# Optimization experiments

Measured on AMD Instinct MI355X. Metric: run time of the kernel, lower is better.

## Reference

```python
import jax, jax.numpy as jnp
import numpy as np

D_CHAR, D_HID, LEN_VOC = 256, 1024, 512
BSZ, MAX_LEN = 128, 256


def setup_inputs() -> dict:
    key = jax.random.key(0)
    ks = jax.random.split(key, 14)
    s = 1.0 / np.sqrt(D_HID)  # PyTorch RNN/Linear init scale
    u = lambda k, shape: jax.random.uniform(k, shape, jnp.float32, -s, s)
    return {
        "inputs": jax.random.randint(ks[0], (BSZ, MAX_LEN), 0, LEN_VOC),
        "outputs": jax.random.randint(ks[1], (BSZ, MAX_LEN), 0, LEN_VOC),
        "emb": jax.random.normal(ks[2], (LEN_VOC, D_CHAR), jnp.float32),
        "enc_Wih": u(ks[3], (D_HID, D_CHAR)),
        "enc_Whh": u(ks[4], (D_HID, D_HID)),
        "enc_bih": u(ks[5], (D_HID,)),
        "enc_bhh": u(ks[6], (D_HID,)),
        "dec_Wih": u(ks[7], (D_HID, D_CHAR)),
        "dec_Whh": u(ks[8], (D_HID, D_HID)),
        "dec_bih": u(ks[9], (D_HID,)),
        "dec_bhh": u(ks[10], (D_HID,)),
        "out_W": u(ks[11], (LEN_VOC, D_HID)),
        "out_b": u(ks[12], (LEN_VOC,)),
    }


def rnn_scan(x_seq, h0, Wih, Whh, bih, bhh):
    """Elman RNN (tanh), batch_first input [B, T, D] -> (h_T [B,H], all h [T,B,H]).
    h_t = tanh(W_ih x_t + b_ih + W_hh h_{t-1} + b_hh), matching torch.nn.RNN."""
    # Precompute input projection for all timesteps (one big GEMM).
    xp = jnp.einsum('btd,hd->bth', x_seq, Wih) + bih + bhh  # [B,T,H]
    xp = jnp.swapaxes(xp, 0, 1)  # [T,B,H] for scan

    def step(h, x):
        h = jnp.tanh(x + h @ Whh.T)
        return h, h

    hT, hs = jax.lax.scan(step, h0, xp)
    return hT, hs


def reference(inputs, outputs, emb, enc_Wih, enc_Whh, enc_bih, enc_bhh,
              dec_Wih, dec_Whh, dec_bih, dec_bhh, out_W, out_b):
    bsz, max_len = inputs.shape
    # Encoder over input char embeddings, zero initial hidden.
    embs = emb[inputs]  # [B,T,Dc]
    h0 = jnp.zeros((bsz, D_HID), jnp.float32)
    hT, _ = rnn_scan(embs, h0, enc_Wih, enc_Whh, enc_bih, enc_bhh)
    # Teacher-forced decoder: step 0 gets zero input, step t gets emb(outputs[:, t-1]).
    dec_in = jnp.concatenate(
        [jnp.zeros((bsz, 1, D_CHAR), jnp.float32), emb[outputs[:, :-1]]], axis=1)
    _, dec_hs = rnn_scan(dec_in, hT, dec_Wih, dec_Whh, dec_bih, dec_bhh)  # [T,B,H]
    # decoder_states.transpose(0,1).view(-1, d_hid)
    states = jnp.swapaxes(dec_hs, 0, 1).reshape(-1, D_HID)  # [B*T, H]
    logits = states @ out_W.T + out_b  # [B*T, V]
    return jax.nn.log_softmax(logits, axis=1)
```

## Files before the change

kernel.cpp:

```cpp
#include <hip/hip_runtime.h>


typedef short short8 __attribute__((ext_vector_type(8)));
typedef float floatx4 __attribute__((ext_vector_type(4)));
typedef unsigned int uint4v __attribute__((ext_vector_type(4)));

#define WS_HBUF   0ull
#define WS_STATES (2ull << 20)
#define WS_WB     (66ull << 20)

#define HS_STRIDE 1032

__device__ __forceinline__ float bf2f(unsigned short u) {
  union { unsigned u; float f; } x; x.u = ((unsigned)u) << 16; return x.f;
}
__device__ __forceinline__ unsigned short f2bf(float f) {
  union { float f; unsigned u; } x; x.f = f;
  unsigned r = x.u + 0x7FFFu + ((x.u >> 16) & 1u);
  return (unsigned short)(r >> 16);
}

__global__ __launch_bounds__(256) void cvt_kernel(
    const float* __restrict__ src, unsigned short* __restrict__ dst, int n)
{
  const int i = (blockIdx.x * 256 + threadIdx.x) * 4;
  if (i >= n) return;
  const float4 v = *(const float4*)(src + i);
  unsigned short o[4] = {f2bf(v.x), f2bf(v.y), f2bf(v.z), f2bf(v.w)};
  *(uint2*)(dst + i) = *(const uint2*)o;
}

__global__ __launch_bounds__(256) void gemm_bt_kernel(
    const unsigned short* __restrict__ Abase,
    const int mode,
    const unsigned short* __restrict__ Bmat,
    const float* __restrict__ bias0,
    const float* __restrict__ bias1,
    unsigned short* __restrict__ outp_bf,
    float* __restrict__ outp_f,
    const int K, const int N, const int nbn)
{
  __shared__ unsigned short As[64][264];
  __shared__ unsigned short Bs[64][264];
  __shared__ const unsigned short* rowsrc[64];

  const int tid = threadIdx.x;
  const int lane = tid & 63;
  const int wave = tid >> 6;
  const int bn = blockIdx.x % nbn;
  const int bm = blockIdx.x / nbn;
  const int m0 = bm * 64;
  const int j0 = bn * 64;

  if (tid < 64) {
    const int m = m0 + tid;
    const unsigned short* src;
    if (mode == 0) {
      src = Abase + (size_t)m * K;
    } else {
      src = Abase + ((size_t)(m & 255) * 128 + (m >> 8)) * 1024;
    }
    rowsrc[tid] = src;
  }

  const floatx4 zf = {0.f, 0.f, 0.f, 0.f};
  floatx4 acc0 = zf, acc1 = zf, acc2 = zf, acc3 = zf;

  for (int kc = 0; kc < K; kc += 256) {
    __syncthreads();
#pragma unroll
    for (int i = 0; i < 8; ++i) {
      const int idx = i * 256 + tid;
      const int r = idx >> 5;
      const int c = idx & 31;
      const unsigned short* s = rowsrc[r];
      *(short8*)&As[r][c * 8] = *(const short8*)(s + kc + c * 8);
      *(short8*)&Bs[r][c * 8] =
          *(const short8*)(Bmat + (size_t)(j0 + r) * K + kc + c * 8);
    }
    __syncthreads();
    const int ar = 16 * wave + (lane & 15);
    const int kq = (lane >> 4) * 8;
#pragma unroll
    for (int kk = 0; kk < 8; ++kk) {
      const short8 a = *(const short8*)&As[ar][kk * 32 + kq];
      const short8 bv0 = *(const short8*)&Bs[(lane & 15)][kk * 32 + kq];
      acc0 = __builtin_amdgcn_mfma_f32_16x16x32_bf16(a, bv0, acc0, 0, 0, 0);
      const short8 bv1 = *(const short8*)&Bs[16 + (lane & 15)][kk * 32 + kq];
      acc1 = __builtin_amdgcn_mfma_f32_16x16x32_bf16(a, bv1, acc1, 0, 0, 0);
      const short8 bv2 = *(const short8*)&Bs[32 + (lane & 15)][kk * 32 + kq];
      acc2 = __builtin_amdgcn_mfma_f32_16x16x32_bf16(a, bv2, acc2, 0, 0, 0);
      const short8 bv3 = *(const short8*)&Bs[48 + (lane & 15)][kk * 32 + kq];
      acc3 = __builtin_amdgcn_mfma_f32_16x16x32_bf16(a, bv3, acc3, 0, 0, 0);
    }
  }

  float bs[4] = {0.f, 0.f, 0.f, 0.f};
  if (bias0) {
#pragma unroll
    for (int nt = 0; nt < 4; ++nt) {
      const int jj = j0 + nt * 16 + (lane & 15);
      bs[nt] = bias0[jj] + bias1[jj];
    }
  }
  __syncthreads();
  const int rbase = 16 * wave + (lane >> 4) * 4;
  const int cl = lane & 15;

  if (outp_bf) {
#pragma unroll
    for (int i = 0; i < 4; ++i) {
      As[rbase + i][cl]      = f2bf(acc0[i] + bs[0]);
      As[rbase + i][16 + cl] = f2bf(acc1[i] + bs[1]);
      As[rbase + i][32 + cl] = f2bf(acc2[i] + bs[2]);
      As[rbase + i][48 + cl] = f2bf(acc3[i] + bs[3]);
    }
    __syncthreads();
#pragma unroll
    for (int i = 0; i < 2; ++i) {
      const int idx = i * 256 + tid;
      const int r = idx >> 3;
      const int c = idx & 7;
      *(short8*)(outp_bf + (size_t)(m0 + r) * N + j0 + c * 8) =
          *(const short8*)&As[r][c * 8];
    }
  } else {
    float (*Asf)[66] = (float(*)[66]) & As[0][0];
#pragma unroll
    for (int i = 0; i < 4; ++i) {
      Asf[rbase + i][cl]      = acc0[i] + bs[0];
      Asf[rbase + i][16 + cl] = acc1[i] + bs[1];
      Asf[rbase + i][32 + cl] = acc2[i] + bs[2];
      Asf[rbase + i][48 + cl] = acc3[i] + bs[3];
    }
    __syncthreads();
#pragma unroll
    for (int i = 0; i < 4; ++i) {
      const int idx = i * 256 + tid;
      const int r = idx >> 4;
      const int c = idx & 15;
      *(float4*)(outp_f + (size_t)(m0 + r) * N + j0 + c * 4) =
          *(const float4*)&Asf[r][c * 4];
    }
  }
}

__global__ __launch_bounds__(256) void rnn_scan8_kernel(
    const unsigned short* __restrict__ WhhE,
    const unsigned short* __restrict__ WhhD,
    const unsigned short* __restrict__ projE,
    const unsigned short* __restrict__ projD,
    const float* __restrict__ decBih,
    const float* __restrict__ decBhh,
    const int* __restrict__ intoks,
    const int* __restrict__ outtoks,
    unsigned short* __restrict__ hbuf,
    unsigned short* __restrict__ states,
    unsigned int* __restrict__ flags)
{
  __shared__ unsigned short hs[2 * 16 * HS_STRIDE];
  __shared__ int toks[16 * 257];

  const int tid = threadIdx.x;
  const int lane = tid & 63;
  const int wave = tid >> 6;
  const int g = blockIdx.x & 7;
  const int slot = blockIdx.x >> 3;
  const int b0 = g * 16;
  const int q = lane >> 4;
  const int cl = lane & 15;
  const int jwb = slot * 64 + wave * 16;
  const int jq4 = jwb + q * 4;
  unsigned int* grpflags = flags + (size_t)g * 1024;
  const int myflag = (slot * 4 + wave) * 16;

  short8 w[32];
  const floatx4 zf = {0.f, 0.f, 0.f, 0.f};
  const size_t prodoff = (size_t)(b0 + cl) * 1024 + jq4;

  for (int phase = 0; phase < 2; ++phase) {
    const unsigned short* Whh = phase ? WhhD : WhhE;
    const unsigned short* proj = phase ? projD : projE;
    const int* gt = phase ? outtoks : intoks;
    {
      const unsigned short* wp = Whh + (size_t)(jwb + cl) * 1024 + q * 8;
#pragma unroll
      for (int kk = 0; kk < 32; ++kk) w[kk] = *(const short8*)(wp + kk * 32);
    }
    float xb[4] = {0.f, 0.f, 0.f, 0.f};
    if (phase) {
#pragma unroll
      for (int i = 0; i < 4; ++i) xb[i] = decBih[jq4 + i] + decBhh[jq4 + i];
    }
    __syncthreads();
#pragma unroll
    for (int i = 0; i < 16; ++i) {
      const int idx = i * 256 + tid;
      toks[(idx >> 8) * 257 + (idx & 255)] =
          gt[(size_t)(b0 + (idx >> 8)) * 256 + (idx & 255)];
    }
    __syncthreads();

    for (int t = 0; t < 256; ++t) {
      const int s = phase * 256 + t;
      float xpf[4];
      {
        const int tt = phase ? (t > 0 ? t - 1 : 0) : t;
        const int tok = toks[cl * 257 + tt];
        const uint2 xr = *(const uint2*)(proj + (size_t)tok * 1024 + jq4);
        const unsigned short* xs = (const unsigned short*)&xr;
#pragma unroll
        for (int i = 0; i < 4; ++i) xpf[i] = bf2f(xs[i]);
        if (phase && t == 0) {
#pragma unroll
          for (int i = 0; i < 4; ++i) xpf[i] = xb[i];
        }
      }

      unsigned short* hsb = hs + (s & 1) * (16 * HS_STRIDE);
      if (s > 0) {
        const unsigned target = (unsigned)s;
        for (;;) {
          const unsigned f = __hip_atomic_load(&grpflags[lane * 16],
                                               __ATOMIC_RELAXED,
                                               __HIP_MEMORY_SCOPE_AGENT);
          if (__ballot(f < target) == 0ull) break;
          __builtin_amdgcn_s_sleep(1);
        }
        const unsigned short* hrb = hbuf + (size_t)(s & 1) * 131072 + b0 * 1024;
        uint4v p0, p1, p2, p3, p4, p5, p6, p7;
        {
          const unsigned long long a0 = (unsigned long long)(hrb + tid * 8);
          asm volatile(
              "global_load_dwordx4 %0, %8, off sc0 sc1\n\t"
              "global_load_dwordx4 %1, %9, off sc0 sc1\n\t"
              "global_load_dwordx4 %2, %10, off sc0 sc1\n\t"
              "global_load_dwordx4 %3, %11, off sc0 sc1\n\t"
              "global_load_dwordx4 %4, %12, off sc0 sc1\n\t"
              "global_load_dwordx4 %5, %13, off sc0 sc1\n\t"
              "global_load_dwordx4 %6, %14, off sc0 sc1\n\t"
              "global_load_dwordx4 %7, %15, off sc0 sc1\n\t"
              "s_waitcnt vmcnt(0)"
              : "=&v"(p0), "=&v"(p1), "=&v"(p2), "=&v"(p3),
                "=&v"(p4), "=&v"(p5), "=&v"(p6), "=&v"(p7)
              : "v"(a0),            "v"(a0 + 1 * 4096),
                "v"(a0 + 2 * 4096), "v"(a0 + 3 * 4096),
                "v"(a0 + 4 * 4096), "v"(a0 + 5 * 4096),
                "v"(a0 + 6 * 4096), "v"(a0 + 7 * 4096)
              : "memory");
        }
        __builtin_amdgcn_sched_barrier(0);
        {
          uint4v pp[8] = {p0, p1, p2, p3, p4, p5, p6, p7};
#pragma unroll
          for (int c = 0; c < 8; ++c) {
            const int gg = c * 256 + tid;
            *(uint4v*)&hsb[(gg >> 7) * HS_STRIDE + (gg & 127) * 8] = pp[c];
          }
        }
      }
      __builtin_amdgcn_sched_barrier(0);
      asm volatile("s_waitcnt lgkmcnt(0)" ::: "memory");
      __builtin_amdgcn_s_barrier();
      __builtin_amdgcn_sched_barrier(0);
      __builtin_amdgcn_s_setprio(1);

      floatx4 acc0 = zf, acc1 = zf, acc2 = zf, acc3 = zf;
      if (s > 0) {
        const unsigned short* hrow = &hsb[cl * HS_STRIDE + q * 8];
#pragma unroll
        for (int kk = 0; kk < 32; kk += 4) {
          const short8 a0 = *(const short8*)(hrow + (kk + 0) * 32);
          const short8 a1 = *(const short8*)(hrow + (kk + 1) * 32);
          const short8 a2 = *(const short8*)(hrow + (kk + 2) * 32);
          const short8 a3 = *(const short8*)(hrow + (kk + 3) * 32);
          acc0 = __builtin_amdgcn_mfma_f32_16x16x32_bf16(w[kk + 0], a0, acc0, 0, 0, 0);
          acc1 = __builtin_amdgcn_mfma_f32_16x16x32_bf16(w[kk + 1], a1, acc1, 0, 0, 0);
          acc2 = __builtin_amdgcn_mfma_f32_16x16x32_bf16(w[kk + 2], a2, acc2, 0, 0, 0);
          acc3 = __builtin_amdgcn_mfma_f32_16x16x32_bf16(w[kk + 3], a3, acc3, 0, 0, 0);
        }
      }
      unsigned short ob[4];
#pragma unroll
      for (int i = 0; i < 4; ++i) {
        const float pre = acc0[i] + acc1[i] + acc2[i] + acc3[i] + xpf[i];
        const float e = __expf(2.f * pre);
        ob[i] = f2bf(1.f - 2.f / (e + 1.f));
      }
      const unsigned long long obp = *(const unsigned long long*)ob;
      __hip_atomic_store(
          (unsigned long long*)(hbuf + (size_t)((s + 1) & 1) * 131072 + prodoff),
          obp, __ATOMIC_RELAXED, __HIP_MEMORY_SCOPE_AGENT);
      asm volatile("s_waitcnt vmcnt(0)" ::: "memory");
      if (lane == 0)
        __hip_atomic_store(&grpflags[myflag], (unsigned)(s + 1),
                           __ATOMIC_RELAXED, __HIP_MEMORY_SCOPE_AGENT);
      __builtin_amdgcn_s_setprio(0);
      if (phase) {
        __builtin_nontemporal_store(
            obp, (unsigned long long*)(states + (size_t)t * 131072 + prodoff));
      }
    }
  }
}

__global__ __launch_bounds__(256) void logsoftmax_kernel(
    float* __restrict__ logits, const float* __restrict__ outb)
{
  const int row = blockIdx.x * 4 + (threadIdx.x >> 6);
  const int lane = threadIdx.x & 63;
  float* rp = logits + (size_t)row * 512 + lane * 8;
  const float4 a0 = *(const float4*)rp;
  const float4 a1 = *(const float4*)(rp + 4);
  const float4 b0 = *(const float4*)(outb + lane * 8);
  const float4 b1 = *(const float4*)(outb + lane * 8 + 4);
  float v[8] = {a0.x + b0.x, a0.y + b0.y, a0.z + b0.z, a0.w + b0.w,
                a1.x + b1.x, a1.y + b1.y, a1.z + b1.z, a1.w + b1.w};
  float mx = v[0];
#pragma unroll
  for (int i = 1; i < 8; ++i) mx = fmaxf(mx, v[i]);
#pragma unroll
  for (int m = 1; m < 64; m <<= 1) mx = fmaxf(mx, __shfl_xor(mx, m, 64));
  float sum = 0.f;
#pragma unroll
  for (int i = 0; i < 8; ++i) sum += __expf(v[i] - mx);
#pragma unroll
  for (int m = 1; m < 64; m <<= 1) sum += __shfl_xor(sum, m, 64);
  const float lse = mx + __logf(sum);
  float4 o0 = {v[0] - lse, v[1] - lse, v[2] - lse, v[3] - lse};
  float4 o1 = {v[4] - lse, v[5] - lse, v[6] - lse, v[7] - lse};
  *(float4*)rp = o0;
  *(float4*)(rp + 4) = o1;
}

extern "C" void kernel_launch(void* const* d_in, const int* in_sizes, int n_in,
                              void* d_out, int out_size, void* d_ws, size_t ws_size,
                              hipStream_t stream)
{
  const int* inputs  = (const int*)d_in[0];
  const int* outputs = (const int*)d_in[1];
  const float* emb    = (const float*)d_in[2];
  const float* encWih = (const float*)d_in[3];
  const float* encWhh = (const float*)d_in[4];
  const float* encBih = (const float*)d_in[5];
  const float* encBhh = (const float*)d_in[6];
  const float* decWih = (const float*)d_in[7];
  const float* decWhh = (const float*)d_in[8];
  const float* decBih = (const float*)d_in[9];
  const float* decBhh = (const float*)d_in[10];
  const float* outW   = (const float*)d_in[11];
  const float* outB   = (const float*)d_in[12];

  char* ws = (char*)d_ws;
  unsigned short* hbuf   = (unsigned short*)(ws + WS_HBUF);
  unsigned short* states = (unsigned short*)(ws + WS_STATES);
  char* wb = ws + WS_WB;
  unsigned short* embB  = (unsigned short*)(wb + 0);
  unsigned short* eWihB = (unsigned short*)(wb + (512ull << 10));
  unsigned short* dWihB = (unsigned short*)(wb + (1ull << 20));
  unsigned short* eWhhB = (unsigned short*)(wb + (2ull << 20));
  unsigned short* dWhhB = (unsigned short*)(wb + (4ull << 20));
  unsigned short* outWB = (unsigned short*)(wb + (6ull << 20));
  unsigned short* projE = (unsigned short*)(wb + (7ull << 20));
  unsigned short* projD = (unsigned short*)(wb + (8ull << 20));
  unsigned int*   flags = (unsigned int*)  (wb + (9ull << 20));
  float* logits = (float*)d_out;

  hipMemsetAsync(flags, 0, 8 * 1024 * sizeof(unsigned int), stream);

  cvt_kernel<<<128, 256, 0, stream>>>(emb, embB, 512 * 256);
  cvt_kernel<<<256, 256, 0, stream>>>(encWih, eWihB, 1024 * 256);
  cvt_kernel<<<256, 256, 0, stream>>>(decWih, dWihB, 1024 * 256);
  cvt_kernel<<<1024, 256, 0, stream>>>(encWhh, eWhhB, 1024 * 1024);
  cvt_kernel<<<1024, 256, 0, stream>>>(decWhh, dWhhB, 1024 * 1024);
  cvt_kernel<<<512, 256, 0, stream>>>(outW, outWB, 512 * 1024);

  gemm_bt_kernel<<<128, 256, 0, stream>>>(embB, 0, eWihB, encBih, encBhh,
                                          projE, nullptr, 256, 1024, 16);
  gemm_bt_kernel<<<128, 256, 0, stream>>>(embB, 0, dWihB, decBih, decBhh,
                                          projD, nullptr, 256, 1024, 16);

  rnn_scan8_kernel<<<128, 256, 0, stream>>>(eWhhB, dWhhB, projE, projD,
                                            decBih, decBhh, inputs, outputs,
                                            hbuf, states, flags);

  gemm_bt_kernel<<<4096, 256, 0, stream>>>(states, 3, outWB, nullptr, nullptr,
                                           nullptr, logits, 1024, 512, 8);
  logsoftmax_kernel<<<8192, 256, 0, stream>>>(logits, outB);
}
```

Before: 1.624 ms.

## Fuse output projection GEMM with bias and log-softmax in one kernel

Replaces the separate output GEMM (64x64 tiles) and log-softmax pass with a kernel where each block computes full 512-wide rows for 64 tokens, keeps the logits in registers, adds the bias, and does the row max/sum reductions across lanes before writing the final log-probabilities with nontemporal stores. This removes the round trip of the fp32 logits through HBM and one kernel launch. In exchange each block reloads all of out_W from L2 and holds 128 accumulators per thread, which raises register pressure and reduces occupancy.

```diff
diff --git a/kernel.cpp b/kernel.cpp
--- a/kernel.cpp
+++ b/kernel.cpp
@@ -143,6 +143,123 @@
           *(const float4*)&Asf[r][c * 4];
     }
   }
+}
+
+__global__ __launch_bounds__(256) void out_gemm_lsm_kernel(
+    const unsigned short* __restrict__ states,
+    const unsigned short* __restrict__ Bmat,
+    const float* __restrict__ outb,
+    float* __restrict__ outp)
+{
+  __shared__ unsigned short As[64][264];
+  __shared__ unsigned short Bs[64][264];
+  __shared__ const unsigned short* rowsrc[64];
+  __shared__ float obias[512];
+
+  const int tid = threadIdx.x;
+  const int lane = tid & 63;
+  const int wave = tid >> 6;
+  const int m0 = blockIdx.x * 64;
+
+  if (tid < 64) {
+    const int m = m0 + tid;
+    rowsrc[tid] = states + ((size_t)(m & 255) * 128 + (m >> 8)) * 1024;
+  }
+  obias[tid] = outb[tid];
+  obias[256 + tid] = outb[256 + tid];
+
+  const floatx4 zf = {0.f, 0.f, 0.f, 0.f};
+  floatx4 acc[8][4];
+#pragma unroll
+  for (int bn = 0; bn < 8; ++bn)
+#pragma unroll
+    for (int nt = 0; nt < 4; ++nt) acc[bn][nt] = zf;
+
+  const int ar = 16 * wave + (lane & 15);
+  const int kq = (lane >> 4) * 8;
+
+  for (int kc = 0; kc < 1024; kc += 256) {
+    __syncthreads();
+#pragma unroll
+    for (int i = 0; i < 8; ++i) {
+      const int idx = i * 256 + tid;
+      const int r = idx >> 5;
+      const int c = idx & 31;
+      *(short8*)&As[r][c * 8] = *(const short8*)(rowsrc[r] + kc + c * 8);
+    }
+#pragma unroll
+    for (int bn = 0; bn < 8; ++bn) {
+      __syncthreads();
+#pragma unroll
+      for (int i = 0; i < 8; ++i) {
+        const int idx = i * 256 + tid;
+        const int r = idx >> 5;
+        const int c = idx & 31;
+        *(short8*)&Bs[r][c * 8] =
+            *(const short8*)(Bmat + (size_t)(bn * 64 + r) * 1024 + kc + c * 8);
+      }
+      __syncthreads();
+#pragma unroll
+      for (int kk = 0; kk < 8; ++kk) {
+        const short8 a = *(const short8*)&As[ar][kk * 32 + kq];
+        const short8 bv0 = *(const short8*)&Bs[(lane & 15)][kk * 32 + kq];
+        acc[bn][0] = __builtin_amdgcn_mfma_f32_16x16x32_bf16(a, bv0, acc[bn][0], 0, 0, 0);
+        const short8 bv1 = *(const short8*)&Bs[16 + (lane & 15)][kk * 32 + kq];
+        acc[bn][1] = __builtin_amdgcn_mfma_f32_16x16x32_bf16(a, bv1, acc[bn][1], 0, 0, 0);
+        const short8 bv2 = *(const short8*)&Bs[32 + (lane & 15)][kk * 32 + kq];
+        acc[bn][2] = __builtin_amdgcn_mfma_f32_16x16x32_bf16(a, bv2, acc[bn][2], 0, 0, 0);
+        const short8 bv3 = *(const short8*)&Bs[48 + (lane & 15)][kk * 32 + kq];
+        acc[bn][3] = __builtin_amdgcn_mfma_f32_16x16x32_bf16(a, bv3, acc[bn][3], 0, 0, 0);
+      }
+    }
+  }
+
+  const int rbase = 16 * wave + (lane >> 4) * 4;
+  const int cl = lane & 15;
+#pragma unroll
+  for (int bn = 0; bn < 8; ++bn)
+#pragma unroll
+    for (int nt = 0; nt < 4; ++nt) {
+      const float bv = obias[bn * 64 + nt * 16 + cl];
+#pragma unroll
+      for (int i = 0; i < 4; ++i) acc[bn][nt][i] += bv;
+    }
+  float mx[4] = {-1e30f, -1e30f, -1e30f, -1e30f};
+#pragma unroll
+  for (int bn = 0; bn < 8; ++bn)
+#pragma unroll
+    for (int nt = 0; nt < 4; ++nt)
+#pragma unroll
+      for (int i = 0; i < 4; ++i) mx[i] = fmaxf(mx[i], acc[bn][nt][i]);
+#pragma unroll
+  for (int m = 1; m < 16; m <<= 1)
+#pragma unroll
+    for (int i = 0; i < 4; ++i) mx[i] = fmaxf(mx[i], __shfl_xor(mx[i], m, 64));
+  float sm[4] = {0.f, 0.f, 0.f, 0.f};
+#pragma unroll
+  for (int bn = 0; bn < 8; ++bn)
+#pragma unroll
+    for (int nt = 0; nt < 4; ++nt)
+#pragma unroll
+      for (int i = 0; i < 4; ++i) sm[i] += __expf(acc[bn][nt][i] - mx[i]);
+#pragma unroll
+  for (int m = 1; m < 16; m <<= 1)
+#pragma unroll
+    for (int i = 0; i < 4; ++i) sm[i] += __shfl_xor(sm[i], m, 64);
+  float lse[4];
+#pragma unroll
+  for (int i = 0; i < 4; ++i) lse[i] = mx[i] + __logf(sm[i]);
+
+#pragma unroll
+  for (int bn = 0; bn < 8; ++bn)
+#pragma unroll
+    for (int nt = 0; nt < 4; ++nt)
+#pragma unroll
+      for (int i = 0; i < 4; ++i) {
+        __builtin_nontemporal_store(
+            acc[bn][nt][i] - lse[i],
+            outp + (size_t)(m0 + rbase + i) * 512 + bn * 64 + nt * 16 + cl);
+      }
 }
 
 __global__ __launch_bounds__(256) void rnn_scan8_kernel(
@@ -304,35 +421,6 @@
   }
 }
 
-__global__ __launch_bounds__(256) void logsoftmax_kernel(
-    float* __restrict__ logits, const float* __restrict__ outb)
-{
-  const int row = blockIdx.x * 4 + (threadIdx.x >> 6);
-  const int lane = threadIdx.x & 63;
-  float* rp = logits + (size_t)row * 512 + lane * 8;
-  const float4 a0 = *(const float4*)rp;
-  const float4 a1 = *(const float4*)(rp + 4);
-  const float4 b0 = *(const float4*)(outb + lane * 8);
-  const float4 b1 = *(const float4*)(outb + lane * 8 + 4);
-  float v[8] = {a0.x + b0.x, a0.y + b0.y, a0.z + b0.z, a0.w + b0.w,
-                a1.x + b1.x, a1.y + b1.y, a1.z + b1.z, a1.w + b1.w};
-  float mx = v[0];
-#pragma unroll
-  for (int i = 1; i < 8; ++i) mx = fmaxf(mx, v[i]);
-#pragma unroll
-  for (int m = 1; m < 64; m <<= 1) mx = fmaxf(mx, __shfl_xor(mx, m, 64));
-  float sum = 0.f;
-#pragma unroll
-  for (int i = 0; i < 8; ++i) sum += __expf(v[i] - mx);
-#pragma unroll
-  for (int m = 1; m < 64; m <<= 1) sum += __shfl_xor(sum, m, 64);
-  const float lse = mx + __logf(sum);
-  float4 o0 = {v[0] - lse, v[1] - lse, v[2] - lse, v[3] - lse};
-  float4 o1 = {v[4] - lse, v[5] - lse, v[6] - lse, v[7] - lse};
-  *(float4*)rp = o0;
-  *(float4*)(rp + 4) = o1;
-}
-
 extern "C" void kernel_launch(void* const* d_in, const int* in_sizes, int n_in,
                               void* d_out, int out_size, void* d_ws, size_t ws_size,
                               hipStream_t stream)
@@ -384,7 +472,5 @@
                                             decBih, decBhh, inputs, outputs,
                                             hbuf, states, flags);
 
-  gemm_bt_kernel<<<4096, 256, 0, stream>>>(states, 3, outWB, nullptr, nullptr,
-                                           nullptr, logits, 1024, 512, 8);
-  logsoftmax_kernel<<<8192, 256, 0, stream>>>(logits, outB);
-}
+  out_gemm_lsm_kernel<<<512, 256, 0, stream>>>(states, outWB, outB, logits);
+}
```

Measured after the change: 1.690 ms. +4.0%, slower.
